# Optimization experiments

Hardware: AMD Instinct MI355X
Metric: run time of the kernel (lower is better)

The kernel has to match this reference:

```python
import math
import jax, jax.numpy as jnp
import numpy as np

B, S, D_MODEL, H = 2, 2048, 1024, 16
HEAD_DIM = D_MODEL // H
NUM_BUCKETS = 32
MAX_DISTANCE = 128
SCALING = HEAD_DIM ** (-0.5)


def setup_inputs() -> dict:
    key = jax.random.key(0)
    ks = jax.random.split(key, 6)
    inp = {
        "hidden_states": jax.random.normal(ks[0], (B, S, D_MODEL), jnp.float32),
        "Wq": jax.random.normal(ks[1], (D_MODEL, D_MODEL), jnp.float32) * (D_MODEL ** -0.5),
        "Wk": jax.random.normal(ks[2], (D_MODEL, D_MODEL), jnp.float32) * (D_MODEL ** -0.5),
        "Wv": jax.random.normal(ks[3], (D_MODEL, D_MODEL), jnp.float32) * (D_MODEL ** -0.5),
        "Wo": jax.random.normal(ks[4], (D_MODEL, D_MODEL), jnp.float32) * (D_MODEL ** -0.5),
        "rel_emb": jax.random.normal(ks[5], (NUM_BUCKETS, H), jnp.float32),
    }
    return inp


def _relative_position_bucket(relative_position, num_buckets=NUM_BUCKETS, max_distance=MAX_DISTANCE):
    # bidirectional (encoder) bucketing, matches T5 _relative_position_bucket
    num_buckets = num_buckets // 2
    relative_buckets = (relative_position > 0).astype(jnp.int32) * num_buckets
    relative_position = jnp.abs(relative_position)
    max_exact = num_buckets // 2
    is_small = relative_position < max_exact
    rp_f = jnp.maximum(relative_position, 1).astype(jnp.float32)  # guard log(0)
    rel_if_large = max_exact + (
        jnp.log(rp_f / max_exact) / math.log(max_distance / max_exact) * (num_buckets - max_exact)
    ).astype(jnp.int32)
    rel_if_large = jnp.minimum(rel_if_large, num_buckets - 1)
    relative_buckets = relative_buckets + jnp.where(is_small, relative_position, rel_if_large)
    return relative_buckets


def compute_bias(rel_emb, q_len, k_len):
    context_position = jnp.arange(q_len)[:, None]
    memory_position = jnp.arange(k_len)[None, :]
    relative_position = memory_position - context_position  # [q, k]
    buckets = _relative_position_bucket(relative_position)
    values = rel_emb[buckets]                  # [q, k, H]
    return jnp.transpose(values, (2, 0, 1))[None]  # [1, H, q, k]


def reference(hidden_states, Wq, Wk, Wv, Wo, rel_emb):
    b, s, _ = hidden_states.shape

    def shape(x):  # [b, s, d_model] -> [b, H, s, head_dim]
        return x.reshape(b, s, H, HEAD_DIM).transpose(0, 2, 1, 3)

    q = shape(hidden_states @ Wq.T)
    k = shape(hidden_states @ Wk.T)
    v = shape(hidden_states @ Wv.T)

    position_bias = compute_bias(rel_emb, s, s)            # [1, H, s, s]
    scores = jnp.einsum("bhqd,bhkd->bhqk", q, k) * SCALING + position_bias
    attn = jax.nn.softmax(scores, axis=-1)
    ctx = jnp.einsum("bhqk,bhkd->bhqd", attn, v)           # [b, H, s, head_dim]
    ctx = ctx.transpose(0, 2, 1, 3).reshape(b, s, D_MODEL)
    return ctx @ Wo.T
```

## Files before the change

### kernel.cpp

```cpp
#include <hip/hip_runtime.h>
#include <math.h>

#define H_    16
#define S_    2048
#define DH_   64
#define DM_   1024
#define NTOK_ 4096
#define NBIAS_ 4095

typedef __attribute__((ext_vector_type(8))) short short8;
typedef __attribute__((ext_vector_type(4))) float f32x4;

#define MFMA16(a, b, c) __builtin_amdgcn_mfma_f32_16x16x32_bf16((a), (b), (c), 0, 0, 0)

__device__ __forceinline__ ushort f2bf(float f) {
  union { float f; unsigned u; } x; x.f = f;
  unsigned r = (x.u + 0x7FFFu + ((x.u >> 16) & 1u)) >> 16;
  return (ushort)r;
}
__device__ __forceinline__ ushort f2bf_fast(float f) {
  union { float f; unsigned u; } x; x.f = f;
  return (ushort)((x.u + 0x8000u) >> 16);
}

__device__ __forceinline__ void ldg16_lds(const ushort* g, ushort* l) {
  __builtin_amdgcn_global_load_lds(
      (const __attribute__((address_space(1))) unsigned int*)g,
      (__attribute__((address_space(3))) unsigned int*)l, 16, 0, 0);
}

__global__ void cast_bf16_k(const float* __restrict__ in, ushort* __restrict__ out, int n) {
  int i = (blockIdx.x * blockDim.x + threadIdx.x) * 4;
  if (i >= n) return;
  const float4 v = *(const float4*)(in + i);
  ushort4 o;
  o.x = f2bf(v.x); o.y = f2bf(v.y); o.z = f2bf(v.z); o.w = f2bf(v.w);
  *(ushort4*)(out + i) = o;
}

__global__ void build_bias_k(const float* __restrict__ rel_emb, float* __restrict__ biasTab) {
  int d = blockIdx.x * blockDim.x + threadIdx.x;
  if (d >= NBIAS_) return;
  int rp = d - (S_ - 1);
  int ret = (rp > 0) ? 16 : 0;
  int arp = rp < 0 ? -rp : rp;
  int bucket;
  if (arp < 8) {
    bucket = ret + arp;
  } else {
    float t = logf((float)arp * 0.125f);
    t = t / 2.772588722239781f;
    t = t * 8.0f;
    int large = 8 + (int)t;
    if (large > 15) large = 15;
    bucket = ret + large;
  }
  for (int h = 0; h < H_; ++h)
    biasTab[h * NBIAS_ + d] = rel_emb[bucket * H_ + h];
}

__global__ __launch_bounds__(256) void gemm_qkv_k(
    const ushort* __restrict__ X,
    const ushort* __restrict__ Wq, const ushort* __restrict__ Wk, const ushort* __restrict__ Wv,
    ushort* __restrict__ Q, ushort* __restrict__ K, ushort* __restrict__ Vt)
{
  const int z = blockIdx.z;
  const ushort* __restrict__ W = (z == 0) ? Wq : (z == 1) ? Wk : Wv;
  __shared__ __align__(16) ushort As[128 * 32];
  __shared__ __align__(16) ushort Bs[128 * 32];

  const int tid = threadIdx.x;
  const int wave = tid >> 6, lane = tid & 63;
  const int l15 = lane & 15, l4 = lane >> 4;
  const int wm = wave >> 1, wn = wave & 1;
  const int m0 = blockIdx.y * 128;
  const int n0 = blockIdx.x * 128;
  const int srow = lane >> 2, scol = (lane & 3) * 8;

  f32x4 acc[4][4];
#pragma unroll
  for (int mi = 0; mi < 4; ++mi)
#pragma unroll
    for (int ni = 0; ni < 4; ++ni) acc[mi][ni] = (f32x4){0.f, 0.f, 0.f, 0.f};

  for (int k0 = 0; k0 < DM_; k0 += 32) {
    __syncthreads();
#pragma unroll
    for (int i = 0; i < 4; ++i) {
      int c = wave * 4 + i;
      if (c < 8)
        ldg16_lds(X + (size_t)(m0 + c * 16 + srow) * DM_ + k0 + scol, &As[c * 512]);
      else
        ldg16_lds(W + (size_t)(n0 + (c - 8) * 16 + srow) * DM_ + k0 + scol, &Bs[(c - 8) * 512]);
    }
    __syncthreads();
    short8 af[4], bfr[4];
#pragma unroll
    for (int mi = 0; mi < 4; ++mi)
      af[mi] = *(const short8*)&As[(wm * 64 + mi * 16 + l15) * 32 + l4 * 8];
#pragma unroll
    for (int ni = 0; ni < 4; ++ni)
      bfr[ni] = *(const short8*)&Bs[(wn * 64 + ni * 16 + l15) * 32 + l4 * 8];
#pragma unroll
    for (int mi = 0; mi < 4; ++mi)
#pragma unroll
      for (int ni = 0; ni < 4; ++ni)
        acc[mi][ni] = MFMA16(af[mi], bfr[ni], acc[mi][ni]);
  }

#pragma unroll
  for (int mi = 0; mi < 4; ++mi)
#pragma unroll
    for (int ni = 0; ni < 4; ++ni)
#pragma unroll
      for (int r = 0; r < 4; ++r) {
        int m = m0 + wm * 64 + mi * 16 + l4 * 4 + r;
        int n = n0 + wn * 64 + ni * 16 + l15;
        int b = m >> 11, s = m & (S_ - 1);
        int h = n >> 6, d = n & 63;
        ushort bv = f2bf(acc[mi][ni][r]);
        if (z == 0)      Q [((size_t)(b * H_ + h) * S_ + s) * DH_ + d] = bv;
        else if (z == 1) K [((size_t)(b * H_ + h) * S_ + s) * DH_ + d] = bv;
        else             Vt[((size_t)(b * H_ + h) * DH_ + d) * S_ + s] = bv;
      }
}

__global__ __launch_bounds__(256) void gemm_out_k(
    const ushort* __restrict__ A, const ushort* __restrict__ W, float* __restrict__ out)
{
  __shared__ __align__(16) ushort As[128 * 32];
  __shared__ __align__(16) ushort Bs[128 * 32];
  const int tid = threadIdx.x;
  const int wave = tid >> 6, lane = tid & 63;
  const int l15 = lane & 15, l4 = lane >> 4;
  const int wm = wave >> 1, wn = wave & 1;
  const int m0 = blockIdx.y * 128;
  const int n0 = blockIdx.x * 128;
  const int srow = lane >> 2, scol = (lane & 3) * 8;

  f32x4 acc[4][4];
#pragma unroll
  for (int mi = 0; mi < 4; ++mi)
#pragma unroll
    for (int ni = 0; ni < 4; ++ni) acc[mi][ni] = (f32x4){0.f, 0.f, 0.f, 0.f};

  for (int k0 = 0; k0 < DM_; k0 += 32) {
    __syncthreads();
#pragma unroll
    for (int i = 0; i < 4; ++i) {
      int c = wave * 4 + i;
      if (c < 8)
        ldg16_lds(A + (size_t)(m0 + c * 16 + srow) * DM_ + k0 + scol, &As[c * 512]);
      else
        ldg16_lds(W + (size_t)(n0 + (c - 8) * 16 + srow) * DM_ + k0 + scol, &Bs[(c - 8) * 512]);
    }
    __syncthreads();
    short8 af[4], bfr[4];
#pragma unroll
    for (int mi = 0; mi < 4; ++mi)
      af[mi] = *(const short8*)&As[(wm * 64 + mi * 16 + l15) * 32 + l4 * 8];
#pragma unroll
    for (int ni = 0; ni < 4; ++ni)
      bfr[ni] = *(const short8*)&Bs[(wn * 64 + ni * 16 + l15) * 32 + l4 * 8];
#pragma unroll
    for (int mi = 0; mi < 4; ++mi)
#pragma unroll
      for (int ni = 0; ni < 4; ++ni)
        acc[mi][ni] = MFMA16(af[mi], bfr[ni], acc[mi][ni]);
  }

#pragma unroll
  for (int mi = 0; mi < 4; ++mi)
#pragma unroll
    for (int ni = 0; ni < 4; ++ni)
#pragma unroll
      for (int r = 0; r < 4; ++r) {
        int m = m0 + wm * 64 + mi * 16 + l4 * 4 + r;
        int n = n0 + wn * 64 + ni * 16 + l15;
        out[(size_t)m * DM_ + n] = acc[mi][ni][r];
      }
}

__global__ __launch_bounds__(256, 4) void attn_k(
    const ushort* __restrict__ Q, const ushort* __restrict__ K, const ushort* __restrict__ Vt,
    const float* __restrict__ biasTab, ushort* __restrict__ Ctx)
{
  __shared__ float brev[2112];
  __shared__ __align__(16) ushort Ks[2][64][32];
  __shared__ __align__(16) ushort Vs[2][64][32];
  __shared__ __align__(16) ushort Ps[4][16 * 72];

  const int tid = threadIdx.x;
  const int wave = tid >> 6, lane = tid & 63;
  const int l15 = lane & 15, l4 = lane >> 4;
  const int bh = blockIdx.y;
  const int h = bh & (H_ - 1);
  const int b = bh >> 4;
  const int qb = blockIdx.x * 64;
  const int q0 = qb + wave * 16;
  const int srow = lane >> 2, scol = (lane & 3) * 8;

  for (int j = tid; j < 2111; j += 256) brev[j] = biasTab[h * NBIAS_ + (4094 - j - qb)];

  const ushort* Qh = Q  + (size_t)bh * S_ * DH_;
  const ushort* Kh = K  + (size_t)bh * S_ * DH_;
  const ushort* Vh = Vt + (size_t)bh * DH_ * S_;

  short8 qf[2];
#pragma unroll
  for (int kk = 0; kk < 2; ++kk)
    qf[kk] = *(const short8*)(Qh + (size_t)(q0 + l15) * DH_ + kk * 32 + l4 * 8);

  short8 ones;
#pragma unroll
  for (int i = 0; i < 8; ++i) ones[i] = (short)0x3F80;

  f32x4 of[4];
#pragma unroll
  for (int nt = 0; nt < 4; ++nt) of[nt] = (f32x4){0.f, 0.f, 0.f, 0.f};
  f32x4 ls = (f32x4){0.f, 0.f, 0.f, 0.f};

  ushort* Pw = &Ps[wave][0];
  const int jb0 = 2047 + wave * 16 + l4 * 4 - l15;

  for (int kt = 0; kt < S_; kt += 64) {
    __syncthreads();
#pragma unroll
    for (int i = 0; i < 2; ++i) {
      int c = wave * 2 + i;
      int kk = c >> 2, rg = c & 3;
      ldg16_lds(Kh + (size_t)(kt + rg * 16 + srow) * DH_ + kk * 32 + scol,
                &Ks[0][0][0] + c * 512);
      ldg16_lds(Vh + (size_t)(rg * 16 + srow) * S_ + kt + kk * 32 + scol,
                &Vs[0][0][0] + c * 512);
    }
    __syncthreads();

    f32x4 sc[4];
#pragma unroll
    for (int nt = 0; nt < 4; ++nt) sc[nt] = (f32x4){0.f, 0.f, 0.f, 0.f};
#pragma unroll
    for (int kk = 0; kk < 2; ++kk)
#pragma unroll
      for (int nt = 0; nt < 4; ++nt) {
        short8 kf = *(const short8*)&Ks[kk][nt * 16 + l15][l4 * 8];
        sc[nt] = MFMA16(qf[kk], kf, sc[nt]);
      }

#pragma unroll
    for (int nt = 0; nt < 4; ++nt) {
      const int jb = jb0 - kt - nt * 16;
#pragma unroll
      for (int r = 0; r < 4; ++r) {
        float p = __expf(sc[nt][r] * 0.125f + brev[jb + r]);
        Pw[(l4 * 4 + r) * 72 + nt * 16 + l15] = f2bf_fast(p);
      }
    }

#pragma unroll
    for (int kk = 0; kk < 2; ++kk) {
      short8 pf = *(const short8*)&Pw[l15 * 72 + kk * 32 + l4 * 8];
      ls = MFMA16(pf, ones, ls);
#pragma unroll
      for (int nt = 0; nt < 4; ++nt) {
        short8 vf = *(const short8*)&Vs[kk][nt * 16 + l15][l4 * 8];
        of[nt] = MFMA16(pf, vf, of[nt]);
      }
    }
  }

#pragma unroll
  for (int nt = 0; nt < 4; ++nt)
#pragma unroll
    for (int r = 0; r < 4; ++r) {
      int t = b * S_ + q0 + l4 * 4 + r;
      float v = of[nt][r] / ls[r];
      Ctx[(size_t)t * DM_ + h * 64 + nt * 16 + l15] = f2bf(v);
    }
}

extern "C" void kernel_launch(void* const* d_in, const int* in_sizes, int n_in,
                              void* d_out, int out_size, void* d_ws, size_t ws_size,
                              hipStream_t stream) {
  const float* hs  = (const float*)d_in[0];
  const float* Wq  = (const float*)d_in[1];
  const float* Wk  = (const float*)d_in[2];
  const float* Wv  = (const float*)d_in[3];
  const float* Wo  = (const float*)d_in[4];
  const float* rel = (const float*)d_in[5];
  float* out = (float*)d_out;

  ushort* Xb  = (ushort*)d_ws;
  ushort* Wqb = Xb  + (size_t)NTOK_ * DM_;
  ushort* Wkb = Wqb + (size_t)DM_ * DM_;
  ushort* Wvb = Wkb + (size_t)DM_ * DM_;
  ushort* Wob = Wvb + (size_t)DM_ * DM_;
  ushort* Qd  = Wob + (size_t)DM_ * DM_;
  ushort* Kd  = Qd  + (size_t)NTOK_ * DM_;
  ushort* Vtd = Kd  + (size_t)NTOK_ * DM_;
  float* biasTab = (float*)(Vtd + (size_t)NTOK_ * DM_);
  ushort* Ctx = Xb;

  cast_bf16_k<<<4096, 256, 0, stream>>>(hs, Xb, NTOK_ * DM_);
  cast_bf16_k<<<1024, 256, 0, stream>>>(Wq, Wqb, DM_ * DM_);
  cast_bf16_k<<<1024, 256, 0, stream>>>(Wk, Wkb, DM_ * DM_);
  cast_bf16_k<<<1024, 256, 0, stream>>>(Wv, Wvb, DM_ * DM_);
  cast_bf16_k<<<1024, 256, 0, stream>>>(Wo, Wob, DM_ * DM_);
  build_bias_k<<<16, 256, 0, stream>>>(rel, biasTab);

  gemm_qkv_k<<<dim3(8, 32, 3), 256, 0, stream>>>(Xb, Wqb, Wkb, Wvb, Qd, Kd, Vtd);
  attn_k<<<dim3(S_ / 64, 2 * H_), 256, 0, stream>>>(Qd, Kd, Vtd, biasTab, Ctx);
  gemm_out_k<<<dim3(8, 32), 256, 0, stream>>>(Ctx, Wob, out);
}
```

Measured before the change: 232.8 us.

## Double attention rows per wave, double-buffer K/V tiles, fuse cast kernels

Each attention wave now handles 32 query rows as two 16-row MFMA tiles, so every K/V fragment read from LDS is used twice. K/V tiles are double-buffered: the next tile's global-to-LDS load is issued before computing on the current one, leaving one barrier per iteration. The LDS bias copy is replaced by direct global reads of a table pre-scaled by log2(e), so softmax can use exp2f with a single fma. The five bf16 cast launches are merged into one kernel. In exchange the attention grid halves to 256 blocks, which lowers occupancy, and register pressure rises.

```diff
diff --git a/kernel.cpp b/kernel.cpp
--- a/kernel.cpp
+++ b/kernel.cpp
@@ -29,10 +29,22 @@
       (__attribute__((address_space(3))) unsigned int*)l, 16, 0, 0);
 }
 
-__global__ void cast_bf16_k(const float* __restrict__ in, ushort* __restrict__ out, int n) {
+__global__ void cast_all_k(const float* __restrict__ hs,
+                           const float* __restrict__ wq, const float* __restrict__ wk,
+                           const float* __restrict__ wv, const float* __restrict__ wo,
+                           ushort* __restrict__ out) {
   int i = (blockIdx.x * blockDim.x + threadIdx.x) * 4;
-  if (i >= n) return;
-  const float4 v = *(const float4*)(in + i);
+  const float* src;
+  int off;
+  if (i < NTOK_ * DM_) {
+    src = hs; off = i;
+  } else {
+    int j = i - NTOK_ * DM_;
+    int w = j >> 20;
+    off = j & ((DM_ * DM_) - 1);
+    src = (w == 0) ? wq : (w == 1) ? wk : (w == 2) ? wv : wo;
+  }
+  const float4 v = *(const float4*)(src + off);
   ushort4 o;
   o.x = f2bf(v.x); o.y = f2bf(v.y); o.z = f2bf(v.z); o.w = f2bf(v.w);
   *(ushort4*)(out + i) = o;
@@ -56,7 +68,7 @@
     bucket = ret + large;
   }
   for (int h = 0; h < H_; ++h)
-    biasTab[h * NBIAS_ + d] = rel_emb[bucket * H_ + h];
+    biasTab[h * NBIAS_ + d] = rel_emb[bucket * H_ + h] * 1.4426950408889634f;
 }
 
 __global__ __launch_bounds__(256) void gemm_qkv_k(
@@ -181,14 +193,13 @@
       }
 }
 
-__global__ __launch_bounds__(256, 4) void attn_k(
+__global__ __launch_bounds__(256, 2) void attn_k(
     const ushort* __restrict__ Q, const ushort* __restrict__ K, const ushort* __restrict__ Vt,
     const float* __restrict__ biasTab, ushort* __restrict__ Ctx)
 {
-  __shared__ float brev[2112];
-  __shared__ __align__(16) ushort Ks[2][64][32];
-  __shared__ __align__(16) ushort Vs[2][64][32];
-  __shared__ __align__(16) ushort Ps[4][16 * 72];
+  __shared__ __align__(16) ushort Ks[2][2][64][32];
+  __shared__ __align__(16) ushort Vs[2][2][64][32];
+  __shared__ __align__(16) ushort Ps[4][2][16 * 72];
 
   const int tid = threadIdx.x;
   const int wave = tid >> 6, lane = tid & 63;
@@ -196,86 +207,128 @@
   const int bh = blockIdx.y;
   const int h = bh & (H_ - 1);
   const int b = bh >> 4;
-  const int qb = blockIdx.x * 64;
-  const int q0 = qb + wave * 16;
+  const int qb = blockIdx.x * 128;
+  const int q0 = qb + wave * 32;
   const int srow = lane >> 2, scol = (lane & 3) * 8;
-
-  for (int j = tid; j < 2111; j += 256) brev[j] = biasTab[h * NBIAS_ + (4094 - j - qb)];
 
   const ushort* Qh = Q  + (size_t)bh * S_ * DH_;
   const ushort* Kh = K  + (size_t)bh * S_ * DH_;
   const ushort* Vh = Vt + (size_t)bh * DH_ * S_;
 
-  short8 qf[2];
-#pragma unroll
-  for (int kk = 0; kk < 2; ++kk)
-    qf[kk] = *(const short8*)(Qh + (size_t)(q0 + l15) * DH_ + kk * 32 + l4 * 8);
+  const float* bpA = biasTab + h * NBIAS_ + 2047 + l15 - (q0 + l4 * 4);
+
+  short8 qfA[2], qfB[2];
+#pragma unroll
+  for (int kk = 0; kk < 2; ++kk) {
+    qfA[kk] = *(const short8*)(Qh + (size_t)(q0 + l15) * DH_ + kk * 32 + l4 * 8);
+    qfB[kk] = *(const short8*)(Qh + (size_t)(q0 + 16 + l15) * DH_ + kk * 32 + l4 * 8);
+  }
 
   short8 ones;
 #pragma unroll
   for (int i = 0; i < 8; ++i) ones[i] = (short)0x3F80;
 
-  f32x4 of[4];
-#pragma unroll
-  for (int nt = 0; nt < 4; ++nt) of[nt] = (f32x4){0.f, 0.f, 0.f, 0.f};
-  f32x4 ls = (f32x4){0.f, 0.f, 0.f, 0.f};
-
-  ushort* Pw = &Ps[wave][0];
-  const int jb0 = 2047 + wave * 16 + l4 * 4 - l15;
-
+  f32x4 ofA[4], ofB[4];
+#pragma unroll
+  for (int nt = 0; nt < 4; ++nt) { ofA[nt] = (f32x4){0.f,0.f,0.f,0.f}; ofB[nt] = (f32x4){0.f,0.f,0.f,0.f}; }
+  f32x4 lsA = (f32x4){0.f,0.f,0.f,0.f}, lsB = (f32x4){0.f,0.f,0.f,0.f};
+
+  ushort* PwA = &Ps[wave][0][0];
+  ushort* PwB = &Ps[wave][1][0];
+
+#pragma unroll
+  for (int i = 0; i < 2; ++i) {
+    int c = wave * 2 + i;
+    int kk = c >> 2, rg = c & 3;
+    ldg16_lds(Kh + (size_t)(rg * 16 + srow) * DH_ + kk * 32 + scol, &Ks[0][0][0][0] + c * 512);
+    ldg16_lds(Vh + (size_t)(rg * 16 + srow) * S_ + kk * 32 + scol, &Vs[0][0][0][0] + c * 512);
+  }
+
+  int cur = 0;
   for (int kt = 0; kt < S_; kt += 64) {
     __syncthreads();
-#pragma unroll
-    for (int i = 0; i < 2; ++i) {
-      int c = wave * 2 + i;
-      int kk = c >> 2, rg = c & 3;
-      ldg16_lds(Kh + (size_t)(kt + rg * 16 + srow) * DH_ + kk * 32 + scol,
-                &Ks[0][0][0] + c * 512);
-      ldg16_lds(Vh + (size_t)(rg * 16 + srow) * S_ + kt + kk * 32 + scol,
-                &Vs[0][0][0] + c * 512);
-    }
-    __syncthreads();
-
-    f32x4 sc[4];
-#pragma unroll
-    for (int nt = 0; nt < 4; ++nt) sc[nt] = (f32x4){0.f, 0.f, 0.f, 0.f};
+
+    float bA[16], b0[4];
+    const float* ptA = bpA + kt;
+#pragma unroll
+    for (int nt = 0; nt < 4; ++nt)
+#pragma unroll
+      for (int r = 0; r < 4; ++r)
+        bA[nt * 4 + r] = ptA[nt * 16 - r];
+#pragma unroll
+    for (int r = 0; r < 4; ++r) b0[r] = ptA[-16 - r];
+
+    if (kt + 64 < S_) {
+#pragma unroll
+      for (int i = 0; i < 2; ++i) {
+        int c = wave * 2 + i;
+        int kk = c >> 2, rg = c & 3;
+        ldg16_lds(Kh + (size_t)(kt + 64 + rg * 16 + srow) * DH_ + kk * 32 + scol,
+                  &Ks[cur ^ 1][0][0][0] + c * 512);
+        ldg16_lds(Vh + (size_t)(rg * 16 + srow) * S_ + kt + 64 + kk * 32 + scol,
+                  &Vs[cur ^ 1][0][0][0] + c * 512);
+      }
+    }
+
+    f32x4 scA[4], scB[4];
+#pragma unroll
+    for (int nt = 0; nt < 4; ++nt) { scA[nt] = (f32x4){0.f,0.f,0.f,0.f}; scB[nt] = (f32x4){0.f,0.f,0.f,0.f}; }
 #pragma unroll
     for (int kk = 0; kk < 2; ++kk)
 #pragma unroll
       for (int nt = 0; nt < 4; ++nt) {
-        short8 kf = *(const short8*)&Ks[kk][nt * 16 + l15][l4 * 8];
-        sc[nt] = MFMA16(qf[kk], kf, sc[nt]);
-      }
-
-#pragma unroll
-    for (int nt = 0; nt < 4; ++nt) {
-      const int jb = jb0 - kt - nt * 16;
+        short8 kf = *(const short8*)&Ks[cur][kk][nt * 16 + l15][l4 * 8];
+        scA[nt] = MFMA16(qfA[kk], kf, scA[nt]);
+        scB[nt] = MFMA16(qfB[kk], kf, scB[nt]);
+      }
+
+#pragma unroll
+    for (int nt = 0; nt < 4; ++nt)
 #pragma unroll
       for (int r = 0; r < 4; ++r) {
-        float p = __expf(sc[nt][r] * 0.125f + brev[jb + r]);
-        Pw[(l4 * 4 + r) * 72 + nt * 16 + l15] = f2bf_fast(p);
-      }
-    }
-
+        float p = exp2f(fmaf(scA[nt][r], 0.1803368801f, bA[nt * 4 + r]));
+        PwA[(l4 * 4 + r) * 72 + nt * 16 + l15] = f2bf_fast(p);
+      }
+#pragma unroll
+    for (int nt = 0; nt < 4; ++nt)
+#pragma unroll
+      for (int r = 0; r < 4; ++r) {
+        float bb = (nt == 0) ? b0[r] : bA[(nt - 1) * 4 + r];
+        float p = exp2f(fmaf(scB[nt][r], 0.1803368801f, bb));
+        PwB[(l4 * 4 + r) * 72 + nt * 16 + l15] = f2bf_fast(p);
+      }
+
+    short8 pfA[2], pfB[2];
 #pragma unroll
     for (int kk = 0; kk < 2; ++kk) {
-      short8 pf = *(const short8*)&Pw[l15 * 72 + kk * 32 + l4 * 8];
-      ls = MFMA16(pf, ones, ls);
+      pfA[kk] = *(const short8*)&PwA[l15 * 72 + kk * 32 + l4 * 8];
+      pfB[kk] = *(const short8*)&PwB[l15 * 72 + kk * 32 + l4 * 8];
+    }
+
+#pragma unroll
+    for (int kk = 0; kk < 2; ++kk) {
+      lsA = MFMA16(pfA[kk], ones, lsA);
+      lsB = MFMA16(pfB[kk], ones, lsB);
 #pragma unroll
       for (int nt = 0; nt < 4; ++nt) {
-        short8 vf = *(const short8*)&Vs[kk][nt * 16 + l15][l4 * 8];
-        of[nt] = MFMA16(pf, vf, of[nt]);
-      }
-    }
-  }
-
+        short8 vf = *(const short8*)&Vs[cur][kk][nt * 16 + l15][l4 * 8];
+        ofA[nt] = MFMA16(pfA[kk], vf, ofA[nt]);
+        ofB[nt] = MFMA16(pfB[kk], vf, ofB[nt]);
+      }
+    }
+    cur ^= 1;
+  }
+
+  float invA[4], invB[4];
+#pragma unroll
+  for (int r = 0; r < 4; ++r) { invA[r] = 1.0f / lsA[r]; invB[r] = 1.0f / lsB[r]; }
 #pragma unroll
   for (int nt = 0; nt < 4; ++nt)
 #pragma unroll
     for (int r = 0; r < 4; ++r) {
-      int t = b * S_ + q0 + l4 * 4 + r;
-      float v = of[nt][r] / ls[r];
-      Ctx[(size_t)t * DM_ + h * 64 + nt * 16 + l15] = f2bf(v);
+      int tA = b * S_ + q0 + l4 * 4 + r;
+      Ctx[(size_t)tA * DM_ + h * 64 + nt * 16 + l15] = f2bf(ofA[nt][r] * invA[r]);
+      Ctx[(size_t)(tA + 16) * DM_ + h * 64 + nt * 16 + l15] = f2bf(ofB[nt][r] * invB[r]);
     }
 }
 
@@ -301,14 +354,10 @@
   float* biasTab = (float*)(Vtd + (size_t)NTOK_ * DM_);
   ushort* Ctx = Xb;
 
-  cast_bf16_k<<<4096, 256, 0, stream>>>(hs, Xb, NTOK_ * DM_);
-  cast_bf16_k<<<1024, 256, 0, stream>>>(Wq, Wqb, DM_ * DM_);
-  cast_bf16_k<<<1024, 256, 0, stream>>>(Wk, Wkb, DM_ * DM_);
-  cast_bf16_k<<<1024, 256, 0, stream>>>(Wv, Wvb, DM_ * DM_);
-  cast_bf16_k<<<1024, 256, 0, stream>>>(Wo, Wob, DM_ * DM_);
+  cast_all_k<<<(NTOK_ * DM_ + 4 * DM_ * DM_) / (4 * 256), 256, 0, stream>>>(hs, Wq, Wk, Wv, Wo, Xb);
   build_bias_k<<<16, 256, 0, stream>>>(rel, biasTab);
 
   gemm_qkv_k<<<dim3(8, 32, 3), 256, 0, stream>>>(Xb, Wqb, Wkb, Wvb, Qd, Kd, Vtd);
-  attn_k<<<dim3(S_ / 64, 2 * H_), 256, 0, stream>>>(Qd, Kd, Vtd, biasTab, Ctx);
+  attn_k<<<dim3(S_ / 128, 2 * H_), 256, 0, stream>>>(Qd, Kd, Vtd, biasTab, Ctx);
   gemm_out_k<<<dim3(8, 32), 256, 0, stream>>>(Ctx, Wob, out);
 }
```

After: 221.4 us. 1.05x faster.
